# Performance work log

Measured on AMD Instinct MI355X. Metric: run time of the kernel, lower is better.

Reference implementation:

```python
import jax, jax.numpy as jnp
import numpy as np

MAX_ITERS = 50
EPS_NORM = 1e-8
EPS_SEP = -1e-6


def setup_inputs() -> dict:
    key = jax.random.key(0)
    k1, k2 = jax.random.split(key)
    pointcloud = jax.random.normal(k1, (200000, 3), dtype=jnp.float32)
    targets = jax.random.normal(k2, (256, 3), dtype=jnp.float32)
    return {"pointcloud": pointcloud, "targets": targets}


def reference(pointcloud, targets):
    # pointcloud: [N, d], targets: [M, d]
    N = pointcloud.shape[0]
    M = targets.shape[0]
    p2 = jnp.sum(pointcloud * pointcloud, axis=1)  # [N]
    t2 = jnp.sum(targets * targets, axis=1)        # [M]

    def step(mask, _):
        # squared euclidean distances [M, N] (argmin identical to cdist argmin)
        d2 = t2[:, None] + p2[None, :] - 2.0 * (targets @ pointcloud.T)
        d2 = jnp.where(mask, d2, jnp.inf)
        closest_idx = jnp.argmin(d2, axis=1)           # [M]
        closest_points = pointcloud[closest_idx]       # [M, d]
        a = closest_points - targets
        a = a / (jnp.linalg.norm(a, axis=1, keepdims=True) + EPS_NORM)
        b = jnp.sum(a * closest_points, axis=1)        # [M]
        dot = a @ pointcloud.T - b[:, None]            # [M, N]
        separated = dot >= EPS_SEP
        mask = mask & ~separated
        return mask, (a, b)

    mask0 = jnp.ones((M, N), dtype=bool)
    _, (a_stack, b_stack) = jax.lax.scan(step, mask0, None, length=MAX_ITERS)
    return a_stack, b_stack  # [MAX_ITERS, M, d], [MAX_ITERS, M]
```

## Files before the change

kernel.cpp:

```cpp
#include <hip/hip_runtime.h>
#include <stdint.h>
#include <math.h>

#pragma clang fp contract(off)

#define BLOCK 1024
#define NW (BLOCK / 64)
#define PT 8
#define PB 4
#define MAX_ITERS 50
#define SOLO_CAP 2048
#define EPS_NORM 1e-8f
#define EPS_SEP (-1e-6f)

__global__ __launch_bounds__(BLOCK) void convex_plane_kernel(
    const float* __restrict__ pc, const float* __restrict__ tg,
    float* __restrict__ out, int N, int M, int CAP, int stepsA)
{
    extern __shared__ uint32_t smem[];
    const int tid  = threadIdx.x;
    const int lane = tid & 63;
    const int wv   = tid >> 6;
    const int m    = blockIdx.x;

    const int maskW = stepsA * (PT * BLOCK / 32);
    uint32_t* mask  = smem;
    int*      list  = (int*)(smem + maskW);
    float*    red_d = (float*)(list + CAP);
    int*      red_i = (int*)(red_d + NW);
    int*      cw    = red_i + NW;
    int*      bcast = cw + NW;
    int*      cnt   = bcast + 2;

    const float tx = tg[3*m+0], ty = tg[3*m+1], tz = tg[3*m+2];
    const float t2 = tx*tx + ty*ty + tz*tz;

    float* out_a = out;
    float* out_b = out + (size_t)MAX_ITERS * (size_t)M * 3;

    auto finish = [&](float dmin, int imin, int mycnt, bool cntFromCursor) -> int2 {
        #pragma unroll
        for (int off = 32; off > 0; off >>= 1) {
            float od = __shfl_down(dmin, off, 64);
            int   oi = __shfl_down(imin, off, 64);
            int   oc = __shfl_down(mycnt, off, 64);
            if (od < dmin || (od == dmin && oi < imin)) { dmin = od; imin = oi; }
            mycnt += oc;
        }
        if (lane == 0) { red_d[wv] = dmin; red_i[wv] = imin; cw[wv] = mycnt; }
        __syncthreads();
        if (wv == 0) {
            float bd = (lane < NW) ? red_d[lane] : INFINITY;
            int   bi = (lane < NW) ? red_i[lane] : 0;
            int   c  = (lane < NW) ? cw[lane]    : 0;
            #pragma unroll
            for (int off = 8; off > 0; off >>= 1) {
                float od = __shfl_down(bd, off, 64);
                int   oi = __shfl_down(bi, off, 64);
                int   oc = __shfl_down(c,  off, 64);
                if (od < bd || (od == bd && oi < bi)) { bd = od; bi = oi; }
                c += oc;
            }
            if (lane == 0) { bcast[0] = bi; bcast[1] = cntFromCursor ? cnt[0] : c; }
        }
        __syncthreads();
        int2 r; r.x = bcast[0]; r.y = bcast[1];
        return r;
    };

    auto scanA = [&](int mode, bool build,
                     float ax, float ay, float az, float b) -> int2 {
        if (tid == 0) cnt[0] = 0;
        __syncthreads();
        float dmin = INFINITY;
        int   imin = 0;
        int   mycnt = 0;
        for (int s = 0; s < stepsA; ++s) {
            const int ib    = s * PT * BLOCK + tid;
            const int wbase = s * (PT * BLOCK / 32);
            uint32_t live = 0;
            if (mode == 2) {
                #pragma unroll
                for (int j = 0; j < PT; ++j) {
                    uint32_t w = mask[wbase + j * (BLOCK / 32) + (tid >> 5)];
                    live |= ((w >> (tid & 31)) & 1u) << j;
                }
            } else {
                #pragma unroll
                for (int j = 0; j < PT; ++j)
                    if (ib + j * BLOCK < N) live |= (1u << j);
            }
            float px[PT], py[PT], pz[PT];
            #pragma unroll
            for (int j = 0; j < PT; ++j) {
                if ((live >> j) & 1u) {
                    const float* p = pc + 3 * (size_t)(ib + j * BLOCK);
                    px[j] = p[0]; py[j] = p[1]; pz[j] = p[2];
                }
            }
            uint32_t keepm = 0;
            #pragma unroll
            for (int j = 0; j < PT; ++j) {
                if ((live >> j) & 1u) {
                    bool keep;
                    if (mode == 0) keep = true;
                    else {
                        float dt = ax*px[j] + ay*py[j] + az*pz[j] - b;
                        keep = (dt < EPS_SEP);
                    }
                    if (keep) {
                        keepm |= (1u << j);
                        float p2 = px[j]*px[j] + py[j]*py[j] + pz[j]*pz[j];
                        float tp = tx*px[j] + ty*py[j] + tz*pz[j];
                        float d2 = t2 + p2 - 2.0f*tp;
                        if (d2 < dmin) { dmin = d2; imin = ib + j * BLOCK; }
                    }
                }
            }
            if (mode != 0) {
                #pragma unroll
                for (int j = 0; j < PT; ++j) {
                    unsigned long long bal = __ballot(((keepm >> j) & 1u) != 0u);
                    const int widx = wbase + j * (BLOCK / 32) + (wv << 1);
                    if (lane == 0)       mask[widx]     = (uint32_t)bal;
                    else if (lane == 32) mask[widx + 1] = (uint32_t)(bal >> 32);
                }
            }
            mycnt += (int)__popc(keepm);
            if (build) {
                int c = (int)__popc(keepm);
                int incl = c;
                #pragma unroll
                for (int off = 1; off < 64; off <<= 1) {
                    int o = __shfl_up(incl, off, 64);
                    if (lane >= off) incl += o;
                }
                const int excl = incl - c;
                const int tot  = __shfl(incl, 63, 64);
                int wb = 0;
                if (lane == 0) wb = atomicAdd(cnt, tot);
                wb = __shfl(wb, 0, 64);
                int pos = wb + excl;
                #pragma unroll
                for (int j = 0; j < PT; ++j) {
                    if ((keepm >> j) & 1u) {
                        if (pos < CAP) list[pos] = ib + j * BLOCK;
                        ++pos;
                    }
                }
            }
        }
        return finish(dmin, imin, mycnt, false);
    };

    auto scanB = [&](int count, float ax, float ay, float az, float b) -> int2 {
        if (tid == 0) cnt[0] = 0;
        __syncthreads();
        float dmin = INFINITY;
        int   imin = 0;
        const int per = BLOCK * PB;
        const int bsteps = (count + per - 1) / per;
        for (int s = 0; s < bsteps; ++s) {
            int jv[PB]; float d2v[PB];
            uint32_t keepm = 0;
            #pragma unroll
            for (int q = 0; q < PB; ++q) {
                const int e = s * per + q * BLOCK + tid;
                if (e < count) {
                    const int j = list[e];
                    jv[q] = j;
                    const float* p = pc + 3 * (size_t)j;
                    float px = p[0], py = p[1], pz = p[2];
                    float dt = ax*px + ay*py + az*pz - b;
                    if (dt < EPS_SEP) {
                        keepm |= (1u << q);
                        float p2 = px*px + py*py + pz*pz;
                        float tp = tx*px + ty*py + tz*pz;
                        d2v[q] = t2 + p2 - 2.0f*tp;
                    }
                }
            }
            __syncthreads();
            int c = (int)__popc(keepm);
            int incl = c;
            #pragma unroll
            for (int off = 1; off < 64; off <<= 1) {
                int o = __shfl_up(incl, off, 64);
                if (lane >= off) incl += o;
            }
            const int excl = incl - c;
            const int tot  = __shfl(incl, 63, 64);
            int wb = 0;
            if (lane == 0) wb = atomicAdd(cnt, tot);
            wb = __shfl(wb, 0, 64);
            int pos = wb + excl;
            #pragma unroll
            for (int q = 0; q < PB; ++q) {
                if ((keepm >> q) & 1u) {
                    list[pos] = jv[q];
                    if (d2v[q] < dmin || (d2v[q] == dmin && jv[q] < imin)) {
                        dmin = d2v[q]; imin = jv[q];
                    }
                    ++pos;
                }
            }
        }
        __syncthreads();
        return finish(dmin, imin, 0, true);
    };

    bool comp = false;
    int2 rc = scanA(0, false, 0.f, 0.f, 0.f, 0.f);
    int idx = rc.x, count = rc.y;

    for (int k = 0; k < MAX_ITERS; ++k) {
        if (comp && count <= SOLO_CAP) {
            if (wv != 0) return;
            for (; k < MAX_ITERS; ++k) {
                const float cx = pc[3*idx+0], cy = pc[3*idx+1], cz = pc[3*idx+2];
                const float vx = cx - tx, vy = cy - ty, vz = cz - tz;
                const float nrm = sqrtf(vx*vx + vy*vy + vz*vz);
                const float den = nrm + EPS_NORM;
                const float ax = vx / den, ay = vy / den, az = vz / den;
                const float b  = ax*cx + ay*cy + az*cz;
                if (count == 0) {
                    for (int q = lane; q < MAX_ITERS - k; q += 64) {
                        const int kk = k + q;
                        const size_t oa = ((size_t)kk * M + m) * 3;
                        out_a[oa+0] = ax; out_a[oa+1] = ay; out_a[oa+2] = az;
                        out_b[(size_t)kk * M + m] = b;
                    }
                    return;
                }
                if (lane == 0) {
                    const size_t oa = ((size_t)k * M + m) * 3;
                    out_a[oa+0] = ax; out_a[oa+1] = ay; out_a[oa+2] = az;
                    out_b[(size_t)k * M + m] = b;
                }
                if (k + 1 < MAX_ITERS) {
                    float dmin = INFINITY; int imin = 0; int wcur = 0;
                    for (int e0 = 0; e0 < count; e0 += 64) {
                        const int e = e0 + lane;
                        bool keep = false; int j = 0; float d2v = 0.f;
                        if (e < count) {
                            j = list[e];
                            const float* p = pc + 3 * (size_t)j;
                            float px = p[0], py = p[1], pz = p[2];
                            float dt = ax*px + ay*py + az*pz - b;
                            if (dt < EPS_SEP) {
                                keep = true;
                                float p2 = px*px + py*py + pz*pz;
                                float tp = tx*px + ty*py + tz*pz;
                                d2v = t2 + p2 - 2.0f*tp;
                            }
                        }
                        unsigned long long bal = __ballot(keep);
                        int pos = wcur + (int)__popcll(bal & ((1ull << lane) - 1ull));
                        if (keep) {
                            list[pos] = j;
                            if (d2v < dmin || (d2v == dmin && j < imin)) {
                                dmin = d2v; imin = j;
                            }
                        }
                        wcur += (int)__popcll(bal);
                    }
                    #pragma unroll
                    for (int off = 32; off > 0; off >>= 1) {
                        float od = __shfl_down(dmin, off, 64);
                        int   oi = __shfl_down(imin, off, 64);
                        if (od < dmin || (od == dmin && oi < imin)) { dmin = od; imin = oi; }
                    }
                    idx = __shfl(imin, 0, 64);
                    count = wcur;
                }
            }
            return;
        }

        const float cx = pc[3*idx+0], cy = pc[3*idx+1], cz = pc[3*idx+2];
        const float vx = cx - tx, vy = cy - ty, vz = cz - tz;
        const float nrm = sqrtf(vx*vx + vy*vy + vz*vz);
        const float den = nrm + EPS_NORM;
        const float ax = vx / den, ay = vy / den, az = vz / den;
        const float b  = ax*cx + ay*cy + az*cz;

        if (count == 0) {
            for (int q = tid; q < MAX_ITERS - k; q += BLOCK) {
                const int kk = k + q;
                const size_t oa = ((size_t)kk * M + m) * 3;
                out_a[oa+0] = ax; out_a[oa+1] = ay; out_a[oa+2] = az;
                out_b[(size_t)kk * M + m] = b;
            }
            return;
        }
        if (tid == 0) {
            const size_t oa = ((size_t)k * M + m) * 3;
            out_a[oa+0] = ax; out_a[oa+1] = ay; out_a[oa+2] = az;
            out_b[(size_t)k * M + m] = b;
        }
        if (k + 1 < MAX_ITERS) {
            if (comp) {
                rc = scanB(count, ax, ay, az, b);
            } else {
                const bool build = (count <= 2 * CAP);
                rc = scanA(k == 0 ? 1 : 2, build, ax, ay, az, b);
                if (build && rc.y <= CAP) comp = true;
            }
            idx = rc.x; count = rc.y;
        }
    }
}

extern "C" void kernel_launch(void* const* d_in, const int* in_sizes, int n_in,
                              void* d_out, int out_size, void* d_ws, size_t ws_size,
                              hipStream_t stream) {
    const float* pc = (const float*)d_in[0];
    const float* tg = (const float*)d_in[1];
    float* out = (float*)d_out;
    const int N = in_sizes[0] / 3;
    const int M = in_sizes[1] / 3;
    const int stepsA = (N + BLOCK * PT - 1) / (BLOCK * PT);
    const size_t maskB  = (size_t)stepsA * (PT * BLOCK / 32) * sizeof(uint32_t);
    const size_t fixedB = NW * (2 * sizeof(int) + sizeof(float)) + 3 * sizeof(int);

    int CAP = 32768;
    size_t smem = maskB + (size_t)CAP * sizeof(int) + fixedB;
    if (hipFuncSetAttribute((const void*)convex_plane_kernel,
                            hipFuncAttributeMaxDynamicSharedMemorySize,
                            (int)smem) != hipSuccess) {
        CAP = 8192;
        smem = maskB + (size_t)CAP * sizeof(int) + fixedB;
    }
    convex_plane_kernel<<<M, BLOCK, smem, stream>>>(pc, tg, out, N, M, CAP, stepsA);
}
```

Baseline: 594.1 us.

## Hoist point loads, cache surviving point coords in LDS for solo wave phase

In scanA, point loads are now unconditional with a clamped index, so all PT loads can be issued up front instead of behind per-lane predicates. scanB first gathers list indices and then issues the dependent coordinate loads in batches, overlapping their latency. The single-wave solo phase copies the surviving points' coordinates into LDS (SoA arrays placed after the list) and compacts them together with the index list, so later iterations avoid scattered global gathers. The build threshold is also raised, and scanA gains a tie-break on index; this risks extra loads of masked points and needs more shared memory, which must fit the allocation.

New measurement: 547.5 us. 1.09x faster.

```diff
diff --git a/kernel.cpp b/kernel.cpp
--- a/kernel.cpp
+++ b/kernel.cpp
@@ -38,6 +38,11 @@
     float* out_a = out;
     float* out_b = out + (size_t)MAX_ITERS * (size_t)M * 3;
 
+    auto ldp = [&](int ip, float& x, float& y, float& z) {
+        const float* p = pc + 3 * (size_t)ip;
+        x = p[0]; y = p[1]; z = p[2];
+    };
+
     auto finish = [&](float dmin, int imin, int mycnt, bool cntFromCursor) -> int2 {
         #pragma unroll
         for (int off = 32; off > 0; off >>= 1) {
@@ -93,10 +98,10 @@
             float px[PT], py[PT], pz[PT];
             #pragma unroll
             for (int j = 0; j < PT; ++j) {
-                if ((live >> j) & 1u) {
-                    const float* p = pc + 3 * (size_t)(ib + j * BLOCK);
-                    px[j] = p[0]; py[j] = p[1]; pz[j] = p[2];
-                }
+                int ip = ib + j * BLOCK;
+                ip = ip < N ? ip : N - 1;
+                const float* p = pc + 3 * (size_t)ip;
+                px[j] = p[0]; py[j] = p[1]; pz[j] = p[2];
             }
             uint32_t keepm = 0;
             #pragma unroll
@@ -113,7 +118,10 @@
                         float p2 = px[j]*px[j] + py[j]*py[j] + pz[j]*pz[j];
                         float tp = tx*px[j] + ty*py[j] + tz*pz[j];
                         float d2 = t2 + p2 - 2.0f*tp;
-                        if (d2 < dmin) { dmin = d2; imin = ib + j * BLOCK; }
+                        const int i = ib + j * BLOCK;
+                        if (d2 < dmin || (d2 == dmin && i < imin)) {
+                            dmin = d2; imin = i;
+                        }
                     }
                 }
             }
@@ -161,21 +169,27 @@
         const int per = BLOCK * PB;
         const int bsteps = (count + per - 1) / per;
         for (int s = 0; s < bsteps; ++s) {
-            int jv[PB]; float d2v[PB];
+            int jv[PB]; float xv[PB], yv[PB], zv[PB];
+            #pragma unroll
+            for (int q = 0; q < PB; ++q) {
+                int e = s * per + q * BLOCK + tid;
+                e = e < count ? e : count - 1;
+                jv[q] = list[e];
+            }
+            #pragma unroll
+            for (int q = 0; q < PB; ++q)
+                ldp(jv[q], xv[q], yv[q], zv[q]);
             uint32_t keepm = 0;
+            float d2v[PB];
             #pragma unroll
             for (int q = 0; q < PB; ++q) {
                 const int e = s * per + q * BLOCK + tid;
                 if (e < count) {
-                    const int j = list[e];
-                    jv[q] = j;
-                    const float* p = pc + 3 * (size_t)j;
-                    float px = p[0], py = p[1], pz = p[2];
-                    float dt = ax*px + ay*py + az*pz - b;
+                    float dt = ax*xv[q] + ay*yv[q] + az*zv[q] - b;
                     if (dt < EPS_SEP) {
                         keepm |= (1u << q);
-                        float p2 = px*px + py*py + pz*pz;
-                        float tp = tx*px + ty*py + tz*pz;
+                        float p2 = xv[q]*xv[q] + yv[q]*yv[q] + zv[q]*zv[q];
+                        float tp = tx*xv[q] + ty*yv[q] + tz*zv[q];
                         d2v[q] = t2 + p2 - 2.0f*tp;
                     }
                 }
@@ -215,9 +229,19 @@
 
     for (int k = 0; k < MAX_ITERS; ++k) {
         if (comp && count <= SOLO_CAP) {
+            float* lx = (float*)(list + SOLO_CAP);
+            float* ly = lx + SOLO_CAP;
+            float* lz = ly + SOLO_CAP;
+            for (int e = tid; e < count; e += BLOCK) {
+                float x, y, z;
+                ldp(list[e], x, y, z);
+                lx[e] = x; ly[e] = y; lz[e] = z;
+            }
+            __syncthreads();
             if (wv != 0) return;
             for (; k < MAX_ITERS; ++k) {
-                const float cx = pc[3*idx+0], cy = pc[3*idx+1], cz = pc[3*idx+2];
+                float cx, cy, cz;
+                ldp(idx, cx, cy, cz);
                 const float vx = cx - tx, vy = cy - ty, vz = cz - tz;
                 const float nrm = sqrtf(vx*vx + vy*vy + vz*vz);
                 const float den = nrm + EPS_NORM;
@@ -241,11 +265,11 @@
                     float dmin = INFINITY; int imin = 0; int wcur = 0;
                     for (int e0 = 0; e0 < count; e0 += 64) {
                         const int e = e0 + lane;
-                        bool keep = false; int j = 0; float d2v = 0.f;
+                        bool keep = false; int j = 0;
+                        float d2v = 0.f, px = 0.f, py = 0.f, pz = 0.f;
                         if (e < count) {
                             j = list[e];
-                            const float* p = pc + 3 * (size_t)j;
-                            float px = p[0], py = p[1], pz = p[2];
+                            px = lx[e]; py = ly[e]; pz = lz[e];
                             float dt = ax*px + ay*py + az*pz - b;
                             if (dt < EPS_SEP) {
                                 keep = true;
@@ -258,6 +282,7 @@
                         int pos = wcur + (int)__popcll(bal & ((1ull << lane) - 1ull));
                         if (keep) {
                             list[pos] = j;
+                            lx[pos] = px; ly[pos] = py; lz[pos] = pz;
                             if (d2v < dmin || (d2v == dmin && j < imin)) {
                                 dmin = d2v; imin = j;
                             }
@@ -277,7 +302,8 @@
             return;
         }
 
-        const float cx = pc[3*idx+0], cy = pc[3*idx+1], cz = pc[3*idx+2];
+        float cx, cy, cz;
+        ldp(idx, cx, cy, cz);
         const float vx = cx - tx, vy = cy - ty, vz = cz - tz;
         const float nrm = sqrtf(vx*vx + vy*vy + vz*vz);
         const float den = nrm + EPS_NORM;
@@ -302,7 +328,7 @@
             if (comp) {
                 rc = scanB(count, ax, ay, az, b);
             } else {
-                const bool build = (count <= 2 * CAP);
+                const bool build = (count <= (5 * CAP) / 2);
                 rc = scanA(k == 0 ? 1 : 2, build, ax, ay, az, b);
                 if (build && rc.y <= CAP) comp = true;
             }
```
